# Kernel tuning notes

Measured on AMD Instinct MI355X. Metric: run time of the kernel, lower is better.

The kernel has to match this reference:

```python
import jax, jax.numpy as jnp
import numpy as np

VOCAB = 50000
E = 128      # embedding_dim (== hidden so layer weights stack)
H = 128      # hidden_features
L = 2        # n_layers
B = 256      # batch
T = 2048     # seq_len


def setup_inputs() -> dict:
    key = jax.random.key(0)
    ks = jax.random.split(key, 8)
    s = 1.0 / np.sqrt(H)
    x = jax.random.randint(ks[0], (B, T), 0, VOCAB)
    lengths = jax.random.randint(ks[1], (B,), 1, T + 1)
    emb = jax.random.normal(ks[2], (VOCAB, E), jnp.float32) * 0.1
    W_ih = jax.random.uniform(ks[3], (L, H, H), jnp.float32, -s, s)
    W_hh = jax.random.uniform(ks[4], (L, H, H), jnp.float32, -s, s)
    b = jax.random.uniform(ks[5], (L, H), jnp.float32, -s, s)
    cls_w = jax.random.uniform(ks[6], (H, 1), jnp.float32, -s, s)
    cls_b = jnp.zeros((1,), jnp.float32)
    return {"x": x, "lengths": lengths, "emb": emb, "W_ih": W_ih,
            "W_hh": W_hh, "b": b, "cls_w": cls_w, "cls_b": cls_b}


def reference(x, lengths, emb, W_ih, W_hh, b, cls_w, cls_b):
    # x: [B, T] right-padded token ids; lengths: [B] valid lengths.
    ex = emb[x]                       # [B, T, E]
    xs = jnp.moveaxis(ex, 1, 0)       # [T, B, E]
    seq = x.shape[1]
    mask = jnp.arange(seq)[:, None] < lengths[None, :]  # [T, B] alive at step t

    n_layers = W_ih.shape[0]

    def step(hid, inp):
        # hid: [L, B, H]; packed-RNN semantics: only alive rows update.
        tok, m = inp                  # [B, E], [B]
        h_in = tok
        new = []
        for l in range(n_layers):
            h = jnp.tanh(h_in @ W_ih[l] + hid[l] @ W_hh[l] + b[l])
            h = jnp.where(m[:, None], h, hid[l])
            new.append(h)
            h_in = h
        return jnp.stack(new), None

    hid0 = jnp.zeros((n_layers, x.shape[0], W_hh.shape[-1]), emb.dtype)
    hid, _ = jax.lax.scan(step, hid0, (xs, mask))
    # final hidden of last layer -> single-logit sigmoid classifier
    out = jax.nn.sigmoid(hid[-1] @ cls_w + cls_b)  # [B, 1]
    return out
```

## Files before the change

### kernel.cpp

```cpp
#include <hip/hip_runtime.h>
#include <math.h>

#define BATCH 256
#define SEQ   2048
#define HID   128
#define NTHR  512
#define VOCAB 50000

typedef _Float16 v2h __attribute__((ext_vector_type(2)));
typedef _Float16 v8h __attribute__((ext_vector_type(8)));
typedef float    v4f __attribute__((ext_vector_type(4)));

template<int CTRL>
__device__ __forceinline__ float dpp_movf(float x) {
    return __builtin_bit_cast(float,
        __builtin_amdgcn_update_dpp(0, __builtin_bit_cast(int, x),
                                    CTRL, 0xF, 0xF, false));
}
__device__ __forceinline__ float quad_reduce(float x) {
    x += dpp_movf<0xB1>(x);
    x += dpp_movf<0x4E>(x);
    return x;
}
__device__ __forceinline__ float fast_rcp(float x) { return __builtin_amdgcn_rcpf(x); }
__device__ __forceinline__ float fast_tanh(float z) {
    float e = __expf(2.0f * z);
    return 1.0f - 2.0f * fast_rcp(e + 1.0f);
}
__device__ __forceinline__ float dot2(v2h a, v2h b, float c) {
    return __builtin_amdgcn_fdot2(a, b, c, false);
}
#define BCH(u) __builtin_bit_cast(v2h, (u))
#define BC8(u) __builtin_bit_cast(v8h, (u))

__global__ __launch_bounds__(NTHR, 2) void emb_proj_kernel(
    const float* __restrict__ emb,
    const float* __restrict__ W_ih,
    const float* __restrict__ bias,
    _Float16*    __restrict__ Y)
{
    const int tid  = threadIdx.x;
    const int wave = tid >> 6;
    const int lane = tid & 63;
    const int j    = wave * 16 + (lane >> 2);
    const int q    = lane & 3;

    __shared__ __align__(16) _Float16 xr[HID];

    v2h w[16];
#pragma unroll
    for (int i = 0; i < 16; ++i) {
        const int k = q * 32 + 2 * i;
        w[i] = v2h{(_Float16)W_ih[k * HID + j], (_Float16)W_ih[(k + 1) * HID + j]};
    }
    const float bj = bias[j];
    const float4* embf4 = (const float4*)emb;

    for (int r = blockIdx.x; r < VOCAB; r += gridDim.x) {
        if (tid < 32) {
            float4 v = embf4[(size_t)r * 32 + tid];
            uint a01 = __builtin_bit_cast(uint, __builtin_amdgcn_cvt_pkrtz(v.x, v.y));
            uint a23 = __builtin_bit_cast(uint, __builtin_amdgcn_cvt_pkrtz(v.z, v.w));
            ((uint2*)&xr[0])[tid] = uint2{a01, a23};
        }
        __syncthreads();
        const uint4* xp = (const uint4*)&xr[0] + q * 4;
        float acc = 0.f;
#pragma unroll
        for (int i = 0; i < 4; ++i) {
            const uint4 xu = xp[i];
            acc = dot2(BCH(xu.x), w[4*i+0], acc);
            acc = dot2(BCH(xu.y), w[4*i+1], acc);
            acc = dot2(BCH(xu.z), w[4*i+2], acc);
            acc = dot2(BCH(xu.w), w[4*i+3], acc);
        }
        acc = quad_reduce(acc) + bj;
        if (q == 0) Y[(size_t)r * HID + j] = (_Float16)acc;
        __syncthreads();
    }
}

__global__ __launch_bounds__(NTHR, 2) void rnn_mfma_kernel(
    const int*      __restrict__ x,
    const int*      __restrict__ lengths,
    const _Float16* __restrict__ Y,
    const float*    __restrict__ W_ih,
    const float*    __restrict__ W_hh,
    const float*    __restrict__ bias,
    const float*    __restrict__ cls_w,
    const float*    __restrict__ cls_b,
    float*          __restrict__ out)
{
    const int b    = blockIdx.x;
    const int tid  = threadIdx.x;
    const int wave = tid >> 6;
    const int lane = tid & 63;
    const int kg   = lane >> 4;
    const int jcol = wave * 16 + (lane & 15);

    __shared__ int xids[SEQ];
    __shared__ __align__(16) _Float16 h0h[2][HID];
    __shared__ __align__(16) _Float16 h1h[2][HID];
    __shared__ __align__(16) float    red[HID];

    const int len   = lengths[b];
    const int lenm1 = len - 1;

    for (int i = tid; i < SEQ; i += NTHR) xids[i] = x[b * SEQ + i];
    if (tid < HID) {
        h0h[0][tid] = (_Float16)0.f; h0h[1][tid] = (_Float16)0.f;
        h1h[0][tid] = (_Float16)0.f; h1h[1][tid] = (_Float16)0.f;
    }

    v8h Bhh0[4], Bih1[4], Bhh1[4];
#pragma unroll
    for (int kt = 0; kt < 4; ++kt) {
        v8h b0v, b1v, b2v;
#pragma unroll
        for (int e = 0; e < 8; ++e) {
            const int k = kt * 32 + kg * 8 + e;
            b0v[e] = (_Float16)W_hh[k * HID + jcol];
            b1v[e] = (_Float16)W_ih[HID * HID + k * HID + jcol];
            b2v[e] = (_Float16)W_hh[HID * HID + k * HID + jcol];
        }
        Bhh0[kt] = b0v; Bih1[kt] = b1v; Bhh1[kt] = b2v;
    }
    const float b1r = bias[HID + jcol];

    __syncthreads();

    _Float16 zA = Y[(size_t)xids[0] * HID + jcol];
    _Float16 zB = Y[(size_t)xids[min(1, lenm1)] * HID + jcol];

    int ph = 0, pf = 0;

#define DO_PHASE(RD, WR, ZREG)                                              \
    {                                                                       \
        const uint4* h0p = (const uint4*)&h0h[RD][0];                       \
        const uint4* h1p = (const uint4*)&h1h[RD][0];                       \
        v8h A0[4], A1[4];                                                   \
        _Pragma("unroll")                                                   \
        for (int kt = 0; kt < 4; ++kt) {                                    \
            A0[kt] = BC8(h0p[kt * 4 + kg]);                                 \
            A1[kt] = BC8(h1p[kt * 4 + kg]);                                 \
        }                                                                   \
        const float zc = (float)ZREG;                                       \
        {                                                                   \
            const int tn = xids[min(ph + 2, lenm1)];                        \
            ZREG = Y[(size_t)tn * HID + jcol];                              \
        }                                                                   \
        v4f c0 = {0.f, 0.f, 0.f, 0.f};                                      \
        v4f c1 = {0.f, 0.f, 0.f, 0.f};                                      \
        _Pragma("unroll")                                                   \
        for (int kt = 0; kt < 4; ++kt)                                      \
            c0 = __builtin_amdgcn_mfma_f32_16x16x32_f16(A0[kt], Bhh0[kt], c0, 0, 0, 0); \
        _Pragma("unroll")                                                   \
        for (int kt = 0; kt < 4; ++kt)                                      \
            c1 = __builtin_amdgcn_mfma_f32_16x16x32_f16(A0[kt], Bih1[kt], c1, 0, 0, 0); \
        _Pragma("unroll")                                                   \
        for (int kt = 0; kt < 4; ++kt)                                      \
            c1 = __builtin_amdgcn_mfma_f32_16x16x32_f16(A1[kt], Bhh1[kt], c1, 0, 0, 0); \
        const float t0 = fast_tanh(c0.x + zc);                              \
        const float t1 = fast_tanh(c1.x + b1r);                             \
        if (kg == 0) {                                                      \
            if (ph < len) h0h[WR][jcol] = (_Float16)t0;                     \
            if (ph >= 1)  h1h[WR][jcol] = (_Float16)t1;                     \
        }                                                                   \
        __syncthreads();                                                    \
    }

    for (;;) {
        DO_PHASE(0, 1, zA)
        ++ph;
        if (ph > len) { pf = 1; break; }
        DO_PHASE(1, 0, zB)
        ++ph;
        if (ph > len) { pf = 0; break; }
    }
#undef DO_PHASE

    if (tid < HID) red[tid] = (float)h1h[pf][tid] * cls_w[tid];
    __syncthreads();
    if (tid == 0) {
        float s = 0.f;
        for (int i = 0; i < HID; ++i) s += red[i];
        s += cls_b[0];
        out[b] = fast_rcp(1.0f + __expf(-s));
    }
}

extern "C" void kernel_launch(void* const* d_in, const int* in_sizes, int n_in,
                              void* d_out, int out_size, void* d_ws, size_t ws_size,
                              hipStream_t stream) {
    const int*   x       = (const int*)  d_in[0];
    const int*   lengths = (const int*)  d_in[1];
    const float* emb     = (const float*)d_in[2];
    const float* W_ih    = (const float*)d_in[3];
    const float* W_hh    = (const float*)d_in[4];
    const float* bias    = (const float*)d_in[5];
    const float* cls_w   = (const float*)d_in[6];
    const float* cls_b   = (const float*)d_in[7];
    float*       out     = (float*)      d_out;

    _Float16* Yws = (_Float16*)d_ws;

    emb_proj_kernel<<<2048, NTHR, 0, stream>>>(emb, W_ih, bias, Yws);
    rnn_mfma_kernel<<<BATCH, NTHR, 0, stream>>>(
        x, lengths, Yws, W_ih, W_hh, bias, cls_w, cls_b, out);
}
```

Before: 804.3 us.

## Process sixteen batch rows per block to fill MFMA tiles

The recurrent kernel now handles 16 batch rows per block, so the 16x16 MFMA tiles carry 16 real rows instead of one useful row. That cuts the grid from 256 blocks to 16. Hidden state is kept in swizzled LDS buffers to avoid bank conflicts. Token ids and embedding projections are prefetched per row from global memory rather than staged in LDS. Each block now loops to the longest length among its 16 rows and adds per-step tanh and store work. The classifier is also parallelised with shuffle reductions, and tanh and sigmoid use exp2.

```diff
diff --git a/kernel.cpp b/kernel.cpp
--- a/kernel.cpp
+++ b/kernel.cpp
@@ -4,10 +4,12 @@
 #define BATCH 256
 #define SEQ   2048
 #define HID   128
-#define NTHR  512
 #define VOCAB 50000
+#define RPB   16
+#define NRB   (BATCH / RPB)
 
 typedef _Float16 v2h __attribute__((ext_vector_type(2)));
+typedef _Float16 v4h __attribute__((ext_vector_type(4)));
 typedef _Float16 v8h __attribute__((ext_vector_type(8)));
 typedef float    v4f __attribute__((ext_vector_type(4)));
 
@@ -23,17 +25,15 @@
     return x;
 }
 __device__ __forceinline__ float fast_rcp(float x) { return __builtin_amdgcn_rcpf(x); }
-__device__ __forceinline__ float fast_tanh(float z) {
-    float e = __expf(2.0f * z);
-    return 1.0f - 2.0f * fast_rcp(e + 1.0f);
-}
 __device__ __forceinline__ float dot2(v2h a, v2h b, float c) {
     return __builtin_amdgcn_fdot2(a, b, c, false);
 }
+__device__ __forceinline__ float fast_tanhf(float z) {
+    return 1.0f - 2.0f * fast_rcp(__builtin_amdgcn_exp2f(z * 2.885390081777927f) + 1.0f);
+}
 #define BCH(u) __builtin_bit_cast(v2h, (u))
-#define BC8(u) __builtin_bit_cast(v8h, (u))
-
-__global__ __launch_bounds__(NTHR, 2) void emb_proj_kernel(
+
+__global__ __launch_bounds__(512, 2) void emb_proj_kernel(
     const float* __restrict__ emb,
     const float* __restrict__ W_ih,
     const float* __restrict__ bias,
@@ -80,7 +80,7 @@
     }
 }
 
-__global__ __launch_bounds__(NTHR, 2) void rnn_mfma_kernel(
+__global__ __launch_bounds__(512, 1) void rnn_batch16_kernel(
     const int*      __restrict__ x,
     const int*      __restrict__ lengths,
     const _Float16* __restrict__ Y,
@@ -91,101 +91,124 @@
     const float*    __restrict__ cls_b,
     float*          __restrict__ out)
 {
-    const int b    = blockIdx.x;
+    const int blk  = blockIdx.x;
     const int tid  = threadIdx.x;
-    const int wave = tid >> 6;
+    const int w    = tid >> 6;
     const int lane = tid & 63;
-    const int kg   = lane >> 4;
-    const int jcol = wave * 16 + (lane & 15);
-
-    __shared__ int xids[SEQ];
-    __shared__ __align__(16) _Float16 h0h[2][HID];
-    __shared__ __align__(16) _Float16 h1h[2][HID];
-    __shared__ __align__(16) float    red[HID];
-
-    const int len   = lengths[b];
-    const int lenm1 = len - 1;
-
-    for (int i = tid; i < SEQ; i += NTHR) xids[i] = x[b * SEQ + i];
-    if (tid < HID) {
-        h0h[0][tid] = (_Float16)0.f; h0h[1][tid] = (_Float16)0.f;
-        h1h[0][tid] = (_Float16)0.f; h1h[1][tid] = (_Float16)0.f;
-    }
+    const int rg   = lane >> 4;
+    const int ln   = lane & 15;
+    const int col  = w * 16 + ln;
+
+    __shared__ __align__(16) _Float16 h0s[2][RPB * HID];
+    __shared__ __align__(16) _Float16 h1s[2][RPB * HID];
+    __shared__ __align__(16) float    clsb[RPB][HID];
+
+    for (int i = tid; i < 2 * RPB * HID; i += 512) {
+        ((_Float16*)h0s)[i] = (_Float16)0.f;
+        ((_Float16*)h1s)[i] = (_Float16)0.f;
+    }
+
+    const int rb = blk * RPB;
+    int len4[4];
+#pragma unroll
+    for (int r = 0; r < 4; ++r) len4[r] = lengths[rb + 4 * rg + r];
+    int Tmax = 0;
+    for (int i = 0; i < RPB; ++i) Tmax = max(Tmax, lengths[rb + i]);
 
     v8h Bhh0[4], Bih1[4], Bhh1[4];
 #pragma unroll
     for (int kt = 0; kt < 4; ++kt) {
-        v8h b0v, b1v, b2v;
 #pragma unroll
         for (int e = 0; e < 8; ++e) {
-            const int k = kt * 32 + kg * 8 + e;
-            b0v[e] = (_Float16)W_hh[k * HID + jcol];
-            b1v[e] = (_Float16)W_ih[HID * HID + k * HID + jcol];
-            b2v[e] = (_Float16)W_hh[HID * HID + k * HID + jcol];
-        }
-        Bhh0[kt] = b0v; Bih1[kt] = b1v; Bhh1[kt] = b2v;
-    }
-    const float b1r = bias[HID + jcol];
+            const int k = kt * 32 + rg * 8 + e;
+            Bhh0[kt][e] = (_Float16)W_hh[k * HID + col];
+            Bih1[kt][e] = (_Float16)W_ih[HID * HID + k * HID + col];
+            Bhh1[kt][e] = (_Float16)W_hh[HID * HID + k * HID + col];
+        }
+    }
+    const float b1c = bias[HID + col];
+
+    const int r0 = rb + 4 * rg;
+    _Float16 yA[4], yB[4]; int tA[4], tB[4];
+#pragma unroll
+    for (int r = 0; r < 4; ++r) {
+        yA[r] = Y[(size_t)x[(r0 + r) * SEQ + 0] * HID + col];
+        yB[r] = Y[(size_t)x[(r0 + r) * SEQ + 1] * HID + col];
+        tA[r] = x[(r0 + r) * SEQ + 2];
+        tB[r] = x[(r0 + r) * SEQ + 3];
+    }
+
+    v4h hp0 = {0,0,0,0}, hp1 = {0,0,0,0};
 
     __syncthreads();
 
-    _Float16 zA = Y[(size_t)xids[0] * HID + jcol];
-    _Float16 zB = Y[(size_t)xids[min(1, lenm1)] * HID + jcol];
-
-    int ph = 0, pf = 0;
-
-#define DO_PHASE(RD, WR, ZREG)                                              \
-    {                                                                       \
-        const uint4* h0p = (const uint4*)&h0h[RD][0];                       \
-        const uint4* h1p = (const uint4*)&h1h[RD][0];                       \
-        v8h A0[4], A1[4];                                                   \
-        _Pragma("unroll")                                                   \
-        for (int kt = 0; kt < 4; ++kt) {                                    \
-            A0[kt] = BC8(h0p[kt * 4 + kg]);                                 \
-            A1[kt] = BC8(h1p[kt * 4 + kg]);                                 \
-        }                                                                   \
-        const float zc = (float)ZREG;                                       \
-        {                                                                   \
-            const int tn = xids[min(ph + 2, lenm1)];                        \
-            ZREG = Y[(size_t)tn * HID + jcol];                              \
-        }                                                                   \
-        v4f c0 = {0.f, 0.f, 0.f, 0.f};                                      \
-        v4f c1 = {0.f, 0.f, 0.f, 0.f};                                      \
-        _Pragma("unroll")                                                   \
-        for (int kt = 0; kt < 4; ++kt)                                      \
+#define PHASE(RD, WR, YR, TR, TT)                                            \
+    {                                                                        \
+        v8h A0[4], A1[4];                                                    \
+        const char* ab0 = (const char*)&h0s[RD][0] + ln * 256;               \
+        const char* ab1 = (const char*)&h1s[RD][0] + ln * 256;               \
+        _Pragma("unroll")                                                    \
+        for (int kt = 0; kt < 4; ++kt) {                                     \
+            const int aoff = (((kt * 4 + rg) ^ ln) & 15) * 16;               \
+            A0[kt] = *(const v8h*)(ab0 + aoff);                              \
+            A1[kt] = *(const v8h*)(ab1 + aoff);                              \
+        }                                                                    \
+        v4f c0 = {0,0,0,0}, c1 = {0,0,0,0};                                  \
+        _Pragma("unroll")                                                    \
+        for (int kt = 0; kt < 4; ++kt)                                       \
             c0 = __builtin_amdgcn_mfma_f32_16x16x32_f16(A0[kt], Bhh0[kt], c0, 0, 0, 0); \
-        _Pragma("unroll")                                                   \
-        for (int kt = 0; kt < 4; ++kt)                                      \
+        _Pragma("unroll")                                                    \
+        for (int kt = 0; kt < 4; ++kt)                                       \
             c1 = __builtin_amdgcn_mfma_f32_16x16x32_f16(A0[kt], Bih1[kt], c1, 0, 0, 0); \
-        _Pragma("unroll")                                                   \
-        for (int kt = 0; kt < 4; ++kt)                                      \
+        _Pragma("unroll")                                                    \
+        for (int kt = 0; kt < 4; ++kt)                                       \
             c1 = __builtin_amdgcn_mfma_f32_16x16x32_f16(A1[kt], Bhh1[kt], c1, 0, 0, 0); \
-        const float t0 = fast_tanh(c0.x + zc);                              \
-        const float t1 = fast_tanh(c1.x + b1r);                             \
-        if (kg == 0) {                                                      \
-            if (ph < len) h0h[WR][jcol] = (_Float16)t0;                     \
-            if (ph >= 1)  h1h[WR][jcol] = (_Float16)t1;                     \
-        }                                                                   \
-        __syncthreads();                                                    \
-    }
-
-    for (;;) {
-        DO_PHASE(0, 1, zA)
-        ++ph;
-        if (ph > len) { pf = 1; break; }
-        DO_PHASE(1, 0, zB)
-        ++ph;
-        if (ph > len) { pf = 0; break; }
-    }
-#undef DO_PHASE
-
-    if (tid < HID) red[tid] = (float)h1h[pf][tid] * cls_w[tid];
+        float yf[4];                                                         \
+        _Pragma("unroll")                                                    \
+        for (int r = 0; r < 4; ++r) yf[r] = (float)YR[r];                    \
+        _Pragma("unroll")                                                    \
+        for (int r = 0; r < 4; ++r) {                                        \
+            const int tok = TR[r];                                           \
+            YR[r] = Y[(size_t)tok * HID + col];                              \
+            const int tnx = (TT + 4 < SEQ) ? (TT + 4) : (SEQ - 1);           \
+            TR[r] = x[(r0 + r) * SEQ + tnx];                                 \
+        }                                                                    \
+        _Pragma("unroll")                                                    \
+        for (int r = 0; r < 4; ++r) {                                        \
+            const int row = 4 * rg + r;                                      \
+            const _Float16 t0 = (_Float16)fast_tanhf(c0[r] + yf[r]);         \
+            const _Float16 t1 = (_Float16)fast_tanhf(c1[r] + b1c);           \
+            const _Float16 n0 = (TT < len4[r]) ? t0 : hp0[r];                \
+            const _Float16 n1 = (TT >= 1 && TT <= len4[r]) ? t1 : hp1[r];    \
+            hp0[r] = n0; hp1[r] = n1;                                        \
+            const int cl   = ((2 * w + (ln >> 3)) ^ row) & 15;               \
+            const int woff = row * 256 + cl * 16 + (ln & 7) * 2;             \
+            *(_Float16*)((char*)&h0s[WR][0] + woff) = n0;                    \
+            *(_Float16*)((char*)&h1s[WR][0] + woff) = n1;                    \
+        }                                                                    \
+        __syncthreads();                                                     \
+    }
+
+    for (int t = 0; t <= Tmax; t += 2) {
+        PHASE(0, 1, yA, tA, t)
+        if (t + 1 <= Tmax) PHASE(1, 0, yB, tB, t + 1)
+    }
+#undef PHASE
+
+#pragma unroll
+    for (int r = 0; r < 4; ++r) clsb[4 * rg + r][col] = (float)hp1[r];
     __syncthreads();
-    if (tid == 0) {
-        float s = 0.f;
-        for (int i = 0; i < HID; ++i) s += red[i];
-        s += cls_b[0];
-        out[b] = fast_rcp(1.0f + __expf(-s));
+    {
+        const int row = tid >> 5, s = tid & 31;
+        const float4 hv = *(const float4*)&clsb[row][4 * s];
+        const float4 wv = *(const float4*)&cls_w[4 * s];
+        float d = hv.x * wv.x + hv.y * wv.y + hv.z * wv.z + hv.w * wv.w;
+#pragma unroll
+        for (int o = 16; o >= 1; o >>= 1) d += __shfl_xor(d, o, 32);
+        if (s == 0) {
+            const float z = d + cls_b[0];
+            out[rb + row] = fast_rcp(1.0f + __builtin_amdgcn_exp2f(-z * 1.4426950408889634f));
+        }
     }
 }
 
@@ -204,7 +227,7 @@
 
     _Float16* Yws = (_Float16*)d_ws;
 
-    emb_proj_kernel<<<2048, NTHR, 0, stream>>>(emb, W_ih, bias, Yws);
-    rnn_mfma_kernel<<<BATCH, NTHR, 0, stream>>>(
+    emb_proj_kernel<<<2048, 512, 0, stream>>>(emb, W_ih, bias, Yws);
+    rnn_batch16_kernel<<<NRB, 512, 0, stream>>>(
         x, lengths, Yws, W_ih, W_hh, bias, cls_w, cls_b, out);
 }
```

After: 1.330 ms. +65.4%, slower.
